# Performance work log

Hardware: AMD Instinct MI355X
Metric: run time of the kernel (lower is better)

The kernel has to match this reference:

```python
import jax, jax.numpy as jnp
import numpy as np

B = 4        # batch_size
S = 128      # input spatial grid size per dim (shape=[128,128,128])
C = 64       # feature channels
N = 500000   # active voxels
K = 2        # kernel_size == stride (non-overlapping sparse max pool)


def setup_inputs() -> dict:
    key = jax.random.key(0)
    kf, kb, ks = jax.random.split(key, 3)
    features = jax.random.normal(kf, (N, C), dtype=jnp.float32)
    b = jax.random.randint(kb, (N, 1), 0, B, dtype=jnp.int32)
    zyx = jax.random.randint(ks, (N, 3), 0, S, dtype=jnp.int32)
    coors = jnp.concatenate([b, zyx], axis=1)  # [N, 4] = (batch, z, y, x)
    return {"features": features, "coors": coors}


def reference(features, coors):
    # Layer 1: sparse 2x2x2/stride-2 max pool == segment-max over output voxel ids.
    S1 = S // K  # 64
    b = coors[:, 0]
    z = coors[:, 1] // K
    y = coors[:, 2] // K
    x = coors[:, 3] // K
    seg = ((b * S1 + z) * S1 + y) * S1 + x  # flat output-site id
    nseg = B * S1 * S1 * S1
    # scatter-max: empty segments become -inf (inactive sites)
    dense = jax.ops.segment_max(features, seg, num_segments=nseg)
    cnt = jax.ops.segment_sum(jnp.ones((N,), jnp.int32), seg, num_segments=nseg)
    mask1 = (cnt > 0).reshape(B, S1, S1, S1)
    dense = dense.reshape(B, S1, S1, S1, C)

    # Layer 2: same pooling on the (now grid-aligned) active sites.
    # -inf at inactive sites makes block-max equal to max over active sites only.
    S2 = S1 // K  # 32
    blocks = dense.reshape(B, S2, K, S2, K, S2, K, C)
    pooled = blocks.max(axis=(2, 4, 6))               # [B, S2, S2, S2, C]
    mask2 = mask1.reshape(B, S2, K, S2, K, S2, K).any(axis=(2, 4, 6))
    out = jnp.where(mask2[..., None], pooled, jnp.float32(0.0))
    return out
```

## Files before the change

kernel.cpp:

```cpp
#include <hip/hip_runtime.h>

#define NB 4
#define S_OUT 32
#define NC 64
#define OUT_CELLS (NB * S_OUT * S_OUT * S_OUT)
#define OUT_ELEMS (OUT_CELLS * NC)
#define NGROUPS (OUT_CELLS / 4)
#define CAP 16
#define OVF_CAP 65536

typedef float floatx4 __attribute__((ext_vector_type(4)));


__global__ __launch_bounds__(256) void zero_kernel(uint4* __restrict__ cnt4,
                                                   int* __restrict__ ovf_cnt) {
    int i = blockIdx.x * blockDim.x + threadIdx.x;
    cnt4[i] = make_uint4(0u, 0u, 0u, 0u);
    if (i == 0) *ovf_cnt = 0;
}

__global__ void fill_kernel(const int4* __restrict__ coors,
                            int* __restrict__ cnt,
                            int* __restrict__ list,
                            int* __restrict__ ovf_cnt,
                            int* __restrict__ ovf,
                            int n_pts) {
    int p = blockIdx.x * blockDim.x + threadIdx.x;
    if (p >= n_pts) return;
    int4 co = coors[p];
    int cell = ((co.x * S_OUT + (co.y >> 2)) * S_OUT + (co.z >> 2)) * S_OUT + (co.w >> 2);
    int slot = atomicAdd(&cnt[cell], 1);
    if (slot < CAP) {
        list[cell * CAP + slot] = p;
    } else {
        int o = atomicAdd(ovf_cnt, 1);
        if (o < OVF_CAP) ovf[o] = p;
    }
}

__global__ __launch_bounds__(256) void gather_kernel(
        const float* __restrict__ features,
        const int4* __restrict__ coors,
        const int* __restrict__ cnt,
        const int* __restrict__ list,
        const int* __restrict__ ovf_cnt,
        const int* __restrict__ ovf,
        float* __restrict__ out) {
    const int lane  = threadIdx.x & 63;
    const int wid   = (blockIdx.x * blockDim.x + threadIdx.x) >> 6;
    const int nw    = (gridDim.x * blockDim.x) >> 6;
    const int cl    = (lane & 15) << 2;
    const int sbase = lane & 48;
    const int qsel  = lane >> 4;

    int g = wid;
    if (g >= NGROUPS) return;

    int n_pf  = cnt[(g << 2) + qsel];
    int pl_pf = list[((size_t)g << 6) + lane];

    while (true) {
        int n  = n_pf;
        int pl = pl_pf;
        int gn = g + nw;
        if (gn < NGROUPS) {
            n_pf  = cnt[(gn << 2) + qsel];
            pl_pf = list[((size_t)gn << 6) + lane];
        }

        int m = n < CAP ? n : CAP;
        float4 acc = make_float4(-INFINITY, -INFINITY, -INFINITY, -INFINITY);

        #pragma unroll
        for (int s = 0; s < 8; ++s) {
            int p = __shfl(pl, sbase + s);
            if (s < m) {
                const float4 f = *(const float4*)(features + (size_t)p * NC + cl);
                acc.x = fmaxf(acc.x, f.x); acc.y = fmaxf(acc.y, f.y);
                acc.z = fmaxf(acc.z, f.z); acc.w = fmaxf(acc.w, f.w);
            }
        }
        if (m > 8) {
            for (int s = 8; s < m; ++s) {
                int p = __shfl(pl, sbase + s);
                const float4 f = *(const float4*)(features + (size_t)p * NC + cl);
                acc.x = fmaxf(acc.x, f.x); acc.y = fmaxf(acc.y, f.y);
                acc.z = fmaxf(acc.z, f.z); acc.w = fmaxf(acc.w, f.w);
            }
        }
        if (__builtin_expect(__any(n > CAP), 0)) {
            int mycell = (g << 2) + qsel;
            int novf = *ovf_cnt;
            if (novf > OVF_CAP) novf = OVF_CAP;
            for (int i = 0; i < novf; ++i) {
                int p = ovf[i];
                int4 co = coors[p];
                int cellp = ((co.x * S_OUT + (co.y >> 2)) * S_OUT + (co.z >> 2)) * S_OUT + (co.w >> 2);
                if (n > CAP && cellp == mycell) {
                    const float4 f = *(const float4*)(features + (size_t)p * NC + cl);
                    acc.x = fmaxf(acc.x, f.x); acc.y = fmaxf(acc.y, f.y);
                    acc.z = fmaxf(acc.z, f.z); acc.w = fmaxf(acc.w, f.w);
                }
            }
        }
        if (n == 0) acc = make_float4(0.f, 0.f, 0.f, 0.f);
        floatx4 accv = { acc.x, acc.y, acc.z, acc.w };
        __builtin_nontemporal_store(accv, (floatx4*)(out + ((size_t)g << 8) + (size_t)lane * 4));

        if (gn >= NGROUPS) break;
        g = gn;
    }
}


__device__ __forceinline__ unsigned flip_f(float f) {
    unsigned u = __float_as_uint(f);
    return (u & 0x80000000u) ? ~u : (u | 0x80000000u);
}
__device__ __forceinline__ float unflip_f(unsigned u) {
    unsigned v = (u & 0x80000000u) ? (u & 0x7FFFFFFFu) : ~u;
    return __uint_as_float(v);
}

__global__ void init_kernel(uint4* __restrict__ out4, int n4) {
    int i = blockIdx.x * blockDim.x + threadIdx.x;
    int stride = gridDim.x * blockDim.x;
    uint4 z = make_uint4(0u, 0u, 0u, 0u);
    for (; i < n4; i += stride) out4[i] = z;
}

__global__ void scatter_kernel(const float* __restrict__ features,
                               const int4* __restrict__ coors,
                               unsigned* __restrict__ acc, int n_pts) {
    int gid = blockIdx.x * blockDim.x + threadIdx.x;
    int p = gid >> 6;
    int c = threadIdx.x & 63;
    if (p >= n_pts) return;
    int4 co = coors[p];
    int cell = ((co.x * S_OUT + (co.y >> 2)) * S_OUT + (co.z >> 2)) * S_OUT + (co.w >> 2);
    atomicMax(acc + (size_t)cell * NC + c, flip_f(features[(size_t)p * NC + c]));
}

__global__ void finalize_kernel(unsigned* __restrict__ acc, int n) {
    int i = blockIdx.x * blockDim.x + threadIdx.x;
    int stride = gridDim.x * blockDim.x;
    for (; i < n; i += stride) {
        unsigned u = acc[i];
        ((float*)acc)[i] = (u == 0u) ? 0.0f : unflip_f(u);
    }
}

extern "C" void kernel_launch(void* const* d_in, const int* in_sizes, int n_in,
                              void* d_out, int out_size, void* d_ws, size_t ws_size,
                              hipStream_t stream) {
    const float* features = (const float*)d_in[0];
    const int4*  coors    = (const int4*)d_in[1];
    int n_pts = in_sizes[0] / NC;

    const size_t off_cnt  = 0;
    const size_t cnt_b    = (size_t)OUT_CELLS * 4;
    const size_t off_ovfc = cnt_b;
    const size_t off_ovf  = off_ovfc + 256;
    const size_t off_list = off_ovf + (size_t)OVF_CAP * 4;
    const size_t need     = off_list + (size_t)OUT_CELLS * CAP * 4;

    if (ws_size >= need) {
        char* ws = (char*)d_ws;
        int* cnt     = (int*)(ws + off_cnt);
        int* ovf_cnt = (int*)(ws + off_ovfc);
        int* ovf     = (int*)(ws + off_ovf);
        int* list    = (int*)(ws + off_list);
        float* out   = (float*)d_out;

        {
            int n4 = OUT_CELLS * 4 / 16;
            zero_kernel<<<n4 / 256, 256, 0, stream>>>((uint4*)cnt, ovf_cnt);
        }
        {
            int block = 256;
            int grid = (n_pts + block - 1) / block;
            fill_kernel<<<grid, block, 0, stream>>>(coors, cnt, list, ovf_cnt, ovf, n_pts);
        }
        {
            int block = 256;
            int grid = 2048;
            gather_kernel<<<grid, block, 0, stream>>>(features, coors, cnt, list,
                                                      ovf_cnt, ovf, out);
        }
    } else {
        unsigned* acc = (unsigned*)d_out;
        init_kernel<<<2048, 256, 0, stream>>>((uint4*)d_out, OUT_ELEMS / 4);
        int grid = (n_pts * 64 + 255) / 256;
        scatter_kernel<<<grid, 256, 0, stream>>>(features, coors, acc, n_pts);
        finalize_kernel<<<2048, 256, 0, stream>>>(acc, OUT_ELEMS);
    }
}
```

Before: 62.10 us.

## Transpose per-cell point lists to slot-major and launch one wave per cell group

The per-cell index list is stored slot-major (slot * cells + cell) instead of cell-major, so the gather reads index s for neighbouring cells contiguously and drops the shuffle broadcast. The persistent grid-stride gather loop with software prefetch is replaced by a full grid with one wavefront per four-cell group. Only slots below each cell's count are read, so the slot-major layout touches fewer cache lines for sparse cells. The trade-offs are scattered writes in the fill kernel and the loss of the prefetch overlap.

Result: slower. 65.35 us (+5.2%).

```diff
diff --git a/kernel.cpp b/kernel.cpp
--- a/kernel.cpp
+++ b/kernel.cpp
@@ -8,6 +8,7 @@
 #define NGROUPS (OUT_CELLS / 4)
 #define CAP 16
 #define OVF_CAP 65536
+#define GATHER_BLOCKS (NGROUPS / 4)
 
 typedef float floatx4 __attribute__((ext_vector_type(4)));
 
@@ -21,7 +22,7 @@
 
 __global__ void fill_kernel(const int4* __restrict__ coors,
                             int* __restrict__ cnt,
-                            int* __restrict__ list,
+                            int* __restrict__ list_t,
                             int* __restrict__ ovf_cnt,
                             int* __restrict__ ovf,
                             int n_pts) {
@@ -31,7 +32,7 @@
     int cell = ((co.x * S_OUT + (co.y >> 2)) * S_OUT + (co.z >> 2)) * S_OUT + (co.w >> 2);
     int slot = atomicAdd(&cnt[cell], 1);
     if (slot < CAP) {
-        list[cell * CAP + slot] = p;
+        list_t[slot * OUT_CELLS + cell] = p;
     } else {
         int o = atomicAdd(ovf_cnt, 1);
         if (o < OVF_CAP) ovf[o] = p;
@@ -42,74 +43,53 @@
         const float* __restrict__ features,
         const int4* __restrict__ coors,
         const int* __restrict__ cnt,
-        const int* __restrict__ list,
+        const int* __restrict__ list_t,
         const int* __restrict__ ovf_cnt,
         const int* __restrict__ ovf,
         float* __restrict__ out) {
-    const int lane  = threadIdx.x & 63;
-    const int wid   = (blockIdx.x * blockDim.x + threadIdx.x) >> 6;
-    const int nw    = (gridDim.x * blockDim.x) >> 6;
-    const int cl    = (lane & 15) << 2;
-    const int sbase = lane & 48;
-    const int qsel  = lane >> 4;
+    const int lane = threadIdx.x & 63;
+    const int wid  = (blockIdx.x * blockDim.x + threadIdx.x) >> 6;
+    const int cl   = (lane & 15) << 2;
+    const int cell = (wid << 2) + (lane >> 4);
 
-    int g = wid;
-    if (g >= NGROUPS) return;
+    int n = cnt[cell];
+    int m = n < CAP ? n : CAP;
+    float4 acc = make_float4(-INFINITY, -INFINITY, -INFINITY, -INFINITY);
 
-    int n_pf  = cnt[(g << 2) + qsel];
-    int pl_pf = list[((size_t)g << 6) + lane];
-
-    while (true) {
-        int n  = n_pf;
-        int pl = pl_pf;
-        int gn = g + nw;
-        if (gn < NGROUPS) {
-            n_pf  = cnt[(gn << 2) + qsel];
-            pl_pf = list[((size_t)gn << 6) + lane];
+    #pragma unroll
+    for (int s = 0; s < 8; ++s) {
+        if (s < m) {
+            int p = list_t[s * OUT_CELLS + cell];
+            const float4 f = *(const float4*)(features + (size_t)p * NC + cl);
+            acc.x = fmaxf(acc.x, f.x); acc.y = fmaxf(acc.y, f.y);
+            acc.z = fmaxf(acc.z, f.z); acc.w = fmaxf(acc.w, f.w);
         }
-
-        int m = n < CAP ? n : CAP;
-        float4 acc = make_float4(-INFINITY, -INFINITY, -INFINITY, -INFINITY);
-
-        #pragma unroll
-        for (int s = 0; s < 8; ++s) {
-            int p = __shfl(pl, sbase + s);
-            if (s < m) {
+    }
+    if (__builtin_expect(m > 8, 0)) {
+        for (int s = 8; s < m; ++s) {
+            int p = list_t[s * OUT_CELLS + cell];
+            const float4 f = *(const float4*)(features + (size_t)p * NC + cl);
+            acc.x = fmaxf(acc.x, f.x); acc.y = fmaxf(acc.y, f.y);
+            acc.z = fmaxf(acc.z, f.z); acc.w = fmaxf(acc.w, f.w);
+        }
+    }
+    if (__builtin_expect(__any(n > CAP), 0)) {
+        int novf = *ovf_cnt;
+        if (novf > OVF_CAP) novf = OVF_CAP;
+        for (int i = 0; i < novf; ++i) {
+            int p = ovf[i];
+            int4 co = coors[p];
+            int cellp = ((co.x * S_OUT + (co.y >> 2)) * S_OUT + (co.z >> 2)) * S_OUT + (co.w >> 2);
+            if (n > CAP && cellp == cell) {
                 const float4 f = *(const float4*)(features + (size_t)p * NC + cl);
                 acc.x = fmaxf(acc.x, f.x); acc.y = fmaxf(acc.y, f.y);
                 acc.z = fmaxf(acc.z, f.z); acc.w = fmaxf(acc.w, f.w);
             }
         }
-        if (m > 8) {
-            for (int s = 8; s < m; ++s) {
-                int p = __shfl(pl, sbase + s);
-                const float4 f = *(const float4*)(features + (size_t)p * NC + cl);
-                acc.x = fmaxf(acc.x, f.x); acc.y = fmaxf(acc.y, f.y);
-                acc.z = fmaxf(acc.z, f.z); acc.w = fmaxf(acc.w, f.w);
-            }
-        }
-        if (__builtin_expect(__any(n > CAP), 0)) {
-            int mycell = (g << 2) + qsel;
-            int novf = *ovf_cnt;
-            if (novf > OVF_CAP) novf = OVF_CAP;
-            for (int i = 0; i < novf; ++i) {
-                int p = ovf[i];
-                int4 co = coors[p];
-                int cellp = ((co.x * S_OUT + (co.y >> 2)) * S_OUT + (co.z >> 2)) * S_OUT + (co.w >> 2);
-                if (n > CAP && cellp == mycell) {
-                    const float4 f = *(const float4*)(features + (size_t)p * NC + cl);
-                    acc.x = fmaxf(acc.x, f.x); acc.y = fmaxf(acc.y, f.y);
-                    acc.z = fmaxf(acc.z, f.z); acc.w = fmaxf(acc.w, f.w);
-                }
-            }
-        }
-        if (n == 0) acc = make_float4(0.f, 0.f, 0.f, 0.f);
-        floatx4 accv = { acc.x, acc.y, acc.z, acc.w };
-        __builtin_nontemporal_store(accv, (floatx4*)(out + ((size_t)g << 8) + (size_t)lane * 4));
-
-        if (gn >= NGROUPS) break;
-        g = gn;
     }
+    if (n == 0) acc = make_float4(0.f, 0.f, 0.f, 0.f);
+    floatx4 accv = { acc.x, acc.y, acc.z, acc.w };
+    __builtin_nontemporal_store(accv, (floatx4*)(out + ((size_t)wid << 8) + (size_t)lane * 4));
 }
 
 
@@ -169,7 +149,7 @@
         int* cnt     = (int*)(ws + off_cnt);
         int* ovf_cnt = (int*)(ws + off_ovfc);
         int* ovf     = (int*)(ws + off_ovf);
-        int* list    = (int*)(ws + off_list);
+        int* list_t  = (int*)(ws + off_list);
         float* out   = (float*)d_out;
 
         {
@@ -179,14 +159,10 @@
         {
             int block = 256;
             int grid = (n_pts + block - 1) / block;
-            fill_kernel<<<grid, block, 0, stream>>>(coors, cnt, list, ovf_cnt, ovf, n_pts);
+            fill_kernel<<<grid, block, 0, stream>>>(coors, cnt, list_t, ovf_cnt, ovf, n_pts);
         }
-        {
-            int block = 256;
-            int grid = 2048;
-            gather_kernel<<<grid, block, 0, stream>>>(features, coors, cnt, list,
-                                                      ovf_cnt, ovf, out);
-        }
+        gather_kernel<<<GATHER_BLOCKS, 256, 0, stream>>>(features, coors, cnt, list_t,
+                                                         ovf_cnt, ovf, out);
     } else {
         unsigned* acc = (unsigned*)d_out;
         init_kernel<<<2048, 256, 0, stream>>>((uint4*)d_out, OUT_ELEMS / 4);
```
